# Performance work log

Measured on AMD Instinct MI355X. Metric: run time of the kernel, lower is better.

Reference implementation:

```python
import jax, jax.numpy as jnp
import numpy as np

B, C, H, W = 8, 128, 64, 64


def setup_inputs() -> dict:
    key = jax.random.key(0)
    ks = jax.random.split(key, 8)
    s = 1.0 / np.sqrt(C)
    return {
        "x1": jax.random.normal(ks[0], (B, C, H, W), dtype=jnp.float32),
        "x2": jax.random.normal(ks[1], (B, C, H, W), dtype=jnp.float32),
        "Wq": jax.random.normal(ks[2], (C, C), dtype=jnp.float32) * s,
        "bq": jax.random.normal(ks[3], (C,), dtype=jnp.float32) * s,
        "Wk": jax.random.normal(ks[4], (C, C), dtype=jnp.float32) * s,
        "bk": jax.random.normal(ks[5], (C,), dtype=jnp.float32) * s,
        "Wv": jax.random.normal(ks[6], (C, C), dtype=jnp.float32) * s,
        "bv": jax.random.normal(ks[7], (C,), dtype=jnp.float32) * s,
    }


def reference(x1, x2, Wq, bq, Wk, bk, Wv, bv):
    b, c, h, w = x1.shape
    n = h * w
    # 1x1 conv == channel matmul per pixel; flatten spatial dims -> [b, c, n]
    x1f = x1.reshape(b, c, n)
    x2f = x2.reshape(b, c, n)
    q = jnp.einsum("oc,bcn->bno", Wq, x1f) + bq[None, None, :]  # [b, n, c]
    k = jnp.einsum("oc,bcn->bon", Wk, x2f) + bk[None, :, None]  # [b, c, n]
    v = jnp.einsum("oc,bcn->bon", Wv, x2f) + bv[None, :, None]  # [b, c, n]
    energy = jnp.einsum("bnc,bcm->bnm", q, k)                   # [b, n, n] (unscaled)
    attention = jax.nn.softmax(energy, axis=-1)
    # out[b,c,i] = sum_j v[b,c,j] * attention[b,i,j]
    out = jnp.einsum("bcj,bij->bci", v, attention)
    return out.reshape(b, c, h, w)
```

## Files before the change

kernel.cpp:

```cpp
#include <hip/hip_runtime.h>

typedef float f4 __attribute__((ext_vector_type(4)));
typedef float f16v __attribute__((ext_vector_type(16)));
typedef _Float16 hf;
typedef __fp16 fp16x2 __attribute__((ext_vector_type(2)));
typedef hf h8 __attribute__((ext_vector_type(8)));
typedef unsigned short ushort_t;
typedef unsigned int uint_t;
typedef uint_t u4 __attribute__((ext_vector_type(4)));

#define BATCH 8
#define CH 128
#define NPIX 4096
#define LOG2E 1.4426950408889634f
#define XSTR 65
#define RESCALE_THR 8.0f

__device__ inline f16v mfma32h(h8 a, h8 b, f16v c) {
    return __builtin_amdgcn_mfma_f32_32x32x16_f16(a, b, c, 0, 0, 0);
}

__device__ inline uint_t pk2h(float a, float b) {
    fp16x2 pp = __builtin_amdgcn_cvt_pkrtz(a, b);
    union { fp16x2 v; uint_t u; } cv;
    cv.v = pp;
    return cv.u;
}

__device__ inline void pl32swap(uint_t& a, uint_t& b) {
    asm("v_permlane32_swap_b32 %0, %1" : "+v"(a), "+v"(b));
}

typedef __attribute__((address_space(3))) uint_t lds_uint;
typedef __attribute__((address_space(1))) const uint_t global_uint;
__device__ inline void dma16(const void* g, void* l) {
    __builtin_amdgcn_global_load_lds((global_uint*)g, (lds_uint*)l, 16, 0, 0);
}

__global__ __launch_bounds__(256) void qkv_kernel(const float* __restrict__ x1,
                                                  const float* __restrict__ x2,
                                                  const float* __restrict__ Wq,
                                                  const float* __restrict__ Wk,
                                                  const float* __restrict__ Wv,
                                                  const float* __restrict__ bq,
                                                  const float* __restrict__ bk,
                                                  const float* __restrict__ bv,
                                                  hf* __restrict__ Qf, hf* __restrict__ Kf,
                                                  hf* __restrict__ Vf) {
    __shared__ __align__(16) float Xs[CH * XSTR];

    int bid = blockIdx.x;
    int m = bid >> 9;
    int rem = bid & 511;
    int b = rem & 7;
    int n0 = (rem >> 3) << 6;

    const float* X = ((m == 0) ? x1 : x2) + (size_t)b * CH * NPIX;
    const float* bias = (m == 0) ? bq : (m == 1) ? bk : bv;

    int tid = threadIdx.x;
#pragma unroll
    for (int r = 0; r < 8; ++r) {
        int c = 16 * r + (tid >> 4);
        int n4 = (tid & 15) << 2;
        f4 v = *(const f4*)&X[(size_t)c * NPIX + n0 + n4];
#pragma unroll
        for (int j = 0; j < 4; ++j) Xs[c * XSTR + n4 + j] = v[j];
    }
    __syncthreads();

    int lane = tid & 63;
    int w = tid >> 6;
    int h = lane >> 5;
    int m32 = lane & 31;
    int o0 = w * 32;

    const float* Wsrc = (m == 0) ? Wq : (m == 1) ? Wk : Wv;
    float wscale = (m == 0) ? LOG2E : 1.0f;
    h8 wf[8];
    {
        const float* wrow = Wsrc + (size_t)(o0 + m32) * CH;
#pragma unroll
        for (int kc = 0; kc < 8; ++kc) {
            f4 a = *(const f4*)&wrow[kc * 16 + h * 8];
            f4 b2 = *(const f4*)&wrow[kc * 16 + h * 8 + 4];
            h8 t;
#pragma unroll
            for (int j = 0; j < 4; ++j) {
                t[j] = (hf)(a[j] * wscale);
                t[4 + j] = (hf)(b2[j] * wscale);
            }
            wf[kc] = t;
        }
    }

    f16v acc[2];
#pragma unroll
    for (int g = 0; g < 2; ++g)
#pragma unroll
        for (int r = 0; r < 16; ++r) acc[g][r] = 0.f;

#pragma unroll
    for (int g = 0; g < 2; ++g) {
        const float* xbase = &Xs[h * 8 * XSTR + g * 32 + m32];
#pragma unroll
        for (int kc = 0; kc < 8; ++kc) {
            h8 xh, xl;
#pragma unroll
            for (int j = 0; j < 8; ++j) {
                float f = xbase[(kc * 16 + j) * XSTR];
                hf hi = (hf)f;
                xh[j] = hi;
                xl[j] = (hf)(f - (float)hi);
            }
            if (m == 2) {
                acc[g] = mfma32h(wf[kc], xh, acc[g]);
                acc[g] = mfma32h(wf[kc], xl, acc[g]);
            } else {
                acc[g] = mfma32h(xh, wf[kc], acc[g]);
                acc[g] = mfma32h(xl, wf[kc], acc[g]);
            }
        }
    }

    if (m < 2) {
        float bval = bias[o0 + m32] * ((m == 0) ? LOG2E : 1.0f);
        hf* Y = ((m == 0) ? Qf : Kf) + (size_t)b * NPIX * CH;
#pragma unroll
        for (int g = 0; g < 2; ++g)
#pragma unroll
            for (int r = 0; r < 16; ++r) {
                int n = n0 + g * 32 + (r & 3) + 8 * (r >> 2) + 4 * h;
                Y[(size_t)n * CH + o0 + m32] = (hf)(acc[g][r] + bval);
            }
    } else {
        hf* Yv = Vf + (size_t)b * CH * NPIX;
#pragma unroll
        for (int g = 0; g < 2; ++g)
#pragma unroll
            for (int r = 0; r < 16; ++r) {
                int o = o0 + (r & 3) + 8 * (r >> 2) + 4 * h;
                Yv[(size_t)o * NPIX + n0 + g * 32 + m32] = (hf)(acc[g][r] + bias[o]);
            }
    }
}

__global__ __launch_bounds__(256, 3) void attn_kernel(const hf* __restrict__ Qf,
                                                      const hf* __restrict__ Kf,
                                                      const hf* __restrict__ Vf,
                                                      hf* __restrict__ Opart,
                                                      float* __restrict__ Mpart,
                                                      float* __restrict__ Lpart) {
    __shared__ __align__(16) ushort_t smem[16384];

    int tid = threadIdx.x;
    int lane = tid & 63;
    int w = tid >> 6;
    int h = lane >> 5;
    int m32 = lane & 31;

    int idx = blockIdx.x;
    int b = idx & 7;
    int ks = (idx >> 3) & 3;
    int qt = idx >> 5;
    int q0 = (qt << 7) + w * 32;
    int k0g = ks << 10;

    const hf* Qb = Qf + (size_t)b * NPIX * CH;
    const hf* Kb = Kf + (size_t)b * NPIX * CH;
    const hf* Vb = Vf + (size_t)b * CH * NPIX;

    h8 qf[8];
#pragma unroll
    for (int kc = 0; kc < 8; ++kc)
        qf[kc] = *(const h8*)&Qb[(size_t)(q0 + m32) * CH + kc * 16 + h * 8];

    const hf* pK[2];
    const hf* pV[2];
#pragma unroll
    for (int a = 0; a < 2; ++a) {
        int chunk_hi = w * 2 + a;
        int rowk = chunk_hi * 4 + (lane >> 4);
        int lck = (lane & 15) ^ (rowk & 15);
        pK[a] = Kb + (size_t)(k0g + rowk) * CH + lck * 8;
        int rowv = chunk_hi * 16 + (lane >> 2);
        int lcv = (lane & 3) ^ (rowv & 3);
        pV[a] = Vb + (size_t)rowv * NPIX + k0g + lcv * 8;
    }

#pragma unroll
    for (int a = 0; a < 2; ++a) {
        dma16(pK[a], &smem[(w * 2 + a) * 512]);
        dma16(pV[a], &smem[8192 + (w * 2 + a) * 512]);
        pK[a] += 32 * CH;
        pV[a] += 32;
    }

    f16v accO[4];
#pragma unroll
    for (int ct = 0; ct < 4; ++ct)
#pragma unroll
        for (int r = 0; r < 16; ++r) accO[ct][r] = 0.f;
    float mprev = -1e30f;
    float lsum = 0.f;

    int pvs[2];
#pragma unroll
    for (int g2 = 0; g2 < 2; ++g2) pvs[g2] = (g2 * 2 + h) ^ (m32 & 3);

    __syncthreads();

    for (int t = 0; t < 32; ++t) {
        int cur = t & 1;
        if (t < 31) {
            int nb = 1 - cur;
#pragma unroll
            for (int a = 0; a < 2; ++a) {
                dma16(pK[a], &smem[nb * 4096 + (w * 2 + a) * 512]);
                dma16(pV[a], &smem[8192 + nb * 4096 + (w * 2 + a) * 512]);
                pK[a] += 32 * CH;
                pV[a] += 32;
            }
        }
        const ushort_t* kb = smem + cur * 4096;
        const ushort_t* vb = smem + 8192 + cur * 4096;

        f16v acc;
#pragma unroll
        for (int r = 0; r < 16; ++r) acc[r] = 0.f;
        __builtin_amdgcn_s_setprio(1);
#pragma unroll
        for (int kc = 0; kc < 8; ++kc) {
            int pA = (kc * 2 + h) ^ (m32 & 15);
            h8 ahi = *(const h8*)&kb[m32 * 128 + pA * 8];
            acc = mfma32h(ahi, qf[kc], acc);
        }
        __builtin_amdgcn_s_setprio(0);

        float ta = fmaxf(fmaxf(acc[0], acc[1]), acc[2]);
        float tb = fmaxf(fmaxf(acc[3], acc[4]), acc[5]);
        ta = fmaxf(fmaxf(ta, acc[6]), acc[7]);
        tb = fmaxf(fmaxf(tb, acc[8]), acc[9]);
        ta = fmaxf(fmaxf(ta, acc[10]), acc[11]);
        tb = fmaxf(fmaxf(tb, acc[12]), acc[13]);
        ta = fmaxf(fmaxf(ta, acc[14]), acc[15]);
        float tmax = fmaxf(ta, tb);
        tmax = fmaxf(tmax, __shfl_xor(tmax, 32));
        if (__any(tmax > mprev + RESCALE_THR)) {
            float mnew = fmaxf(mprev, tmax);
            float alpha = exp2f(mprev - mnew);
            lsum *= alpha;
#pragma unroll
            for (int ct = 0; ct < 4; ++ct)
#pragma unroll
                for (int r = 0; r < 16; ++r) accO[ct][r] *= alpha;
            mprev = mnew;
        }

        uint_t pk[8];
        float ps0 = 0.f, ps1 = 0.f;
#pragma unroll
        for (int t2 = 0; t2 < 8; ++t2) {
            float e0 = exp2f(acc[2 * t2] - mprev);
            float e1 = exp2f(acc[2 * t2 + 1] - mprev);
            ps0 += e0;
            ps1 += e1;
            pk[t2] = pk2h(e0, e1);
        }
        float psum = ps0 + ps1;
        psum += __shfl_xor(psum, 32);
        lsum += psum;

        pl32swap(pk[0], pk[2]);
        pl32swap(pk[1], pk[3]);
        pl32swap(pk[4], pk[6]);
        pl32swap(pk[5], pk[7]);
        h8 pbp[2];
#pragma unroll
        for (int g2 = 0; g2 < 2; ++g2) {
            u4 fv;
            fv[0] = pk[g2 * 4 + 0];
            fv[1] = pk[g2 * 4 + 1];
            fv[2] = pk[g2 * 4 + 2];
            fv[3] = pk[g2 * 4 + 3];
            __builtin_memcpy(&pbp[g2], &fv, 16);
        }

        __builtin_amdgcn_s_setprio(1);
#pragma unroll
        for (int g2 = 0; g2 < 2; ++g2) {
            int pv = pvs[g2];
#pragma unroll
            for (int ct = 0; ct < 4; ++ct) {
                h8 av = *(const h8*)&vb[(ct * 32 + m32) * 32 + pv * 8];
                accO[ct] = mfma32h(av, pbp[g2], accO[ct]);
            }
        }
        __builtin_amdgcn_s_setprio(0);

        __syncthreads();
    }

    size_t base = (((size_t)ks * 8 + b) * 32 + qt) * 16384;
    size_t mlb = (((size_t)ks * 8 + b) * 32 + qt) * 128;
    int q = w * 32 + m32;
#pragma unroll
    for (int ct = 0; ct < 4; ++ct)
#pragma unroll
        for (int r = 0; r < 16; ++r) {
            int ch = ct * 32 + (r & 3) + 8 * (r >> 2) + 4 * h;
            Opart[base + ch * 128 + q] = (hf)accO[ct][r];
        }
    if (h == 0) {
        Mpart[mlb + q] = mprev;
        Lpart[mlb + q] = lsum;
    }
}

__global__ __launch_bounds__(256) void combine_kernel(const hf* __restrict__ Opart,
                                                      const float* __restrict__ Mp,
                                                      const float* __restrict__ Lp,
                                                      float* __restrict__ out) {
    int idx = blockIdx.x;
    int chh = idx & 1;
    int b = (idx >> 1) & 7;
    int qt = idx >> 4;
    int tid = threadIdx.x;
    int q8 = (tid & 15) << 3;
    int chl = tid >> 4;

    size_t tile = (size_t)b * 32 + qt;

    float Marr[4][8], Larr[4][8];
#pragma unroll
    for (int p = 0; p < 4; ++p) {
        const float* mp_ = Mp + ((size_t)p * 256 + tile) * 128 + q8;
        const float* lp_ = Lp + ((size_t)p * 256 + tile) * 128 + q8;
        f4 ma = *(const f4*)mp_;
        f4 mb = *(const f4*)(mp_ + 4);
        f4 la = *(const f4*)lp_;
        f4 lb = *(const f4*)(lp_ + 4);
#pragma unroll
        for (int j = 0; j < 4; ++j) {
            Marr[p][j] = ma[j];
            Marr[p][4 + j] = mb[j];
            Larr[p][j] = la[j];
            Larr[p][4 + j] = lb[j];
        }
    }

    float wgt[4][8];
#pragma unroll
    for (int j = 0; j < 8; ++j) {
        float M = fmaxf(fmaxf(Marr[0][j], Marr[1][j]), fmaxf(Marr[2][j], Marr[3][j]));
        float L = 0.f;
#pragma unroll
        for (int p = 0; p < 4; ++p) {
            float w_ = exp2f(Marr[p][j] - M);
            wgt[p][j] = w_;
            L += w_ * Larr[p][j];
        }
        float rd = 1.0f / L;
#pragma unroll
        for (int p = 0; p < 4; ++p) wgt[p][j] *= rd;
    }

    const hf* ob[4];
#pragma unroll
    for (int p = 0; p < 4; ++p) ob[p] = Opart + ((size_t)p * 256 + tile) * 16384 + q8;
    float* O = out + (size_t)b * CH * NPIX + (size_t)qt * 128 + q8;

#pragma unroll
    for (int it = 0; it < 4; ++it) {
        int ch = chh * 64 + it * 16 + chl;
        union { u4 u; h8 v; } o4[4];
#pragma unroll
        for (int p = 0; p < 4; ++p) o4[p].u = *(const u4*)&ob[p][(size_t)ch * 128];
        f4 r0, r1;
#pragma unroll
        for (int j = 0; j < 8; ++j) {
            float s = 0.f;
#pragma unroll
            for (int p = 0; p < 4; ++p) s += wgt[p][j] * (float)o4[p].v[j];
            if (j < 4) r0[j] = s;
            else r1[j - 4] = s;
        }
        float* dst = O + (size_t)ch * NPIX;
        *(f4*)dst = r0;
        *(f4*)(dst + 4) = r1;
    }
}

extern "C" void kernel_launch(void* const* d_in, const int* in_sizes, int n_in,
                              void* d_out, int out_size, void* d_ws, size_t ws_size,
                              hipStream_t stream) {
    const float* x1 = (const float*)d_in[0];
    const float* x2 = (const float*)d_in[1];
    const float* Wq = (const float*)d_in[2];
    const float* bq = (const float*)d_in[3];
    const float* Wk = (const float*)d_in[4];
    const float* bk = (const float*)d_in[5];
    const float* Wv = (const float*)d_in[6];
    const float* bv = (const float*)d_in[7];
    float* outp = (float*)d_out;

    const size_t N = (size_t)BATCH * NPIX * CH;
    hf* Qf = (hf*)d_ws;
    hf* Kf = Qf + N;
    hf* Vf = Qf + 2 * N;
    hf* Opart = Qf + 3 * N;
    float* Mp = (float*)(Opart + (size_t)4 * 8 * 32 * 16384);
    float* Lp = Mp + (size_t)4 * 8 * 32 * 128;

    qkv_kernel<<<3 * BATCH * (NPIX / 64), 256, 0, stream>>>(x1, x2, Wq, Wk, Wv,
                                                            bq, bk, bv, Qf, Kf, Vf);
    attn_kernel<<<BATCH * 4 * (NPIX / 128), 256, 0, stream>>>(Qf, Kf, Vf, Opart, Mp, Lp);
    combine_kernel<<<2 * BATCH * (NPIX / 128), 256, 0, stream>>>(Opart, Mp, Lp, outp);
}
```

Baseline: 214.8 us.

## Pre-split X into fp16 hi/lo swizzled LDS tiles and reswizzle V tile

The QKV projection kernel now converts each input value to an fp16 hi/lo pair once, while staging it, and stores both halves in separate XOR-swizzled LDS arrays laid out pixel-major. This lets each MFMA operand come from a single 16-byte LDS load instead of eight strided scalar float loads plus per-use conversion. The __syncthreads is moved after the weight loads so those overlap with staging. The attention kernel's V tile swizzle gains an extra XOR bit to cut LDS bank conflicts. The new swizzles must agree between DMA writes and reads, and the scalar ushort LDS stores during staging may themselves conflict.

```diff
diff --git a/kernel.cpp b/kernel.cpp
--- a/kernel.cpp
+++ b/kernel.cpp
@@ -13,7 +13,6 @@
 #define CH 128
 #define NPIX 4096
 #define LOG2E 1.4426950408889634f
-#define XSTR 65
 #define RESCALE_THR 8.0f
 
 __device__ inline f16v mfma32h(h8 a, h8 b, f16v c) {
@@ -35,6 +34,12 @@
 typedef __attribute__((address_space(1))) const uint_t global_uint;
 __device__ inline void dma16(const void* g, void* l) {
     __builtin_amdgcn_global_load_lds((global_uint*)g, (lds_uint*)l, 16, 0, 0);
+}
+
+__device__ inline ushort_t h2u(hf x) {
+    union { hf h; ushort_t u; } cv;
+    cv.h = x;
+    return cv.u;
 }
 
 __global__ __launch_bounds__(256) void qkv_kernel(const float* __restrict__ x1,
@@ -47,7 +52,8 @@
                                                   const float* __restrict__ bv,
                                                   hf* __restrict__ Qf, hf* __restrict__ Kf,
                                                   hf* __restrict__ Vf) {
-    __shared__ __align__(16) float Xs[CH * XSTR];
+    __shared__ __align__(16) ushort_t XH[64 * 128];
+    __shared__ __align__(16) ushort_t XL[64 * 128];
 
     int bid = blockIdx.x;
     int m = bid >> 9;
@@ -64,10 +70,17 @@
         int c = 16 * r + (tid >> 4);
         int n4 = (tid & 15) << 2;
         f4 v = *(const f4*)&X[(size_t)c * NPIX + n0 + n4];
-#pragma unroll
-        for (int j = 0; j < 4; ++j) Xs[c * XSTR + n4 + j] = v[j];
-    }
-    __syncthreads();
+        int cs = c >> 3, cj = c & 7;
+#pragma unroll
+        for (int j = 0; j < 4; ++j) {
+            int n = n4 + j;
+            hf hi = (hf)v[j];
+            hf lo = (hf)(v[j] - (float)hi);
+            int ofs = n * 128 + ((cs ^ (n & 15)) << 3) + cj;
+            XH[ofs] = h2u(hi);
+            XL[ofs] = h2u(lo);
+        }
+    }
 
     int lane = tid & 63;
     int w = tid >> 6;
@@ -94,25 +107,23 @@
         }
     }
 
+    __syncthreads();
+
     f16v acc[2];
 #pragma unroll
     for (int g = 0; g < 2; ++g)
 #pragma unroll
         for (int r = 0; r < 16; ++r) acc[g][r] = 0.f;
 
+    int swzn = m32 & 15;
 #pragma unroll
     for (int g = 0; g < 2; ++g) {
-        const float* xbase = &Xs[h * 8 * XSTR + g * 32 + m32];
+        int nrow = (g * 32 + m32) * 128;
 #pragma unroll
         for (int kc = 0; kc < 8; ++kc) {
-            h8 xh, xl;
-#pragma unroll
-            for (int j = 0; j < 8; ++j) {
-                float f = xbase[(kc * 16 + j) * XSTR];
-                hf hi = (hf)f;
-                xh[j] = hi;
-                xl[j] = (hf)(f - (float)hi);
-            }
+            int sofs = nrow + (((kc * 2 + h) ^ swzn) << 3);
+            h8 xh = *(const h8*)&XH[sofs];
+            h8 xl = *(const h8*)&XL[sofs];
             if (m == 2) {
                 acc[g] = mfma32h(wf[kc], xh, acc[g]);
                 acc[g] = mfma32h(wf[kc], xl, acc[g]);
@@ -184,7 +195,7 @@
         int lck = (lane & 15) ^ (rowk & 15);
         pK[a] = Kb + (size_t)(k0g + rowk) * CH + lck * 8;
         int rowv = chunk_hi * 16 + (lane >> 2);
-        int lcv = (lane & 3) ^ (rowv & 3);
+        int lcv = (lane & 3) ^ (rowv & 3) ^ ((rowv >> 2) & 1);
         pV[a] = Vb + (size_t)rowv * NPIX + k0g + lcv * 8;
     }
 
@@ -206,7 +217,8 @@
 
     int pvs[2];
 #pragma unroll
-    for (int g2 = 0; g2 < 2; ++g2) pvs[g2] = (g2 * 2 + h) ^ (m32 & 3);
+    for (int g2 = 0; g2 < 2; ++g2)
+        pvs[g2] = (g2 * 2 + h) ^ (m32 & 3) ^ ((m32 >> 2) & 1);
 
     __syncthreads();
 
```

Result: no change. 210.7 us (-1.9%).
